# Performance work log

Hardware: AMD Instinct MI355X
Metric: run time of the kernel (lower is better)

## Reference

```python
import jax, jax.numpy as jnp
import numpy as np

N_HEADS = 12
HEAD_DIM = 64
EMB_DIM = 768
ATTN_DIM = N_HEADS * HEAD_DIM


def setup_inputs() -> dict:
    key = jax.random.key(0)
    k1, k2, k3, k4 = jax.random.split(key, 4)
    B, N = 8, 1024
    x = jax.random.normal(k1, (B, N, EMB_DIM), dtype=jnp.float32)
    scale = 1.0 / np.sqrt(EMB_DIM)
    w_qkv = jax.random.normal(k2, (EMB_DIM, 3 * ATTN_DIM), dtype=jnp.float32) * scale
    w_out = jax.random.normal(k3, (ATTN_DIM, EMB_DIM), dtype=jnp.float32) * (1.0 / np.sqrt(ATTN_DIM))
    b_out = jax.random.normal(k4, (EMB_DIM,), dtype=jnp.float32) * 0.01
    return {"x": x, "w_qkv": w_qkv, "w_out": w_out, "b_out": b_out}


def reference(x, w_qkv, w_out, b_out):
    B, N, _ = x.shape
    qkv = jnp.einsum('bnd,de->bne', x, w_qkv)  # [B,N,3*attn_dim]
    q, k, v = jnp.split(qkv, 3, axis=-1)
    # [B, n_heads, N, head_dim]
    def heads(t):
        return t.reshape(B, N, N_HEADS, HEAD_DIM).transpose(0, 2, 1, 3)
    q, k, v = heads(q), heads(k), heads(v)
    scores = jnp.einsum('bhnd,bhmd->bhnm', q, k) * (HEAD_DIM ** -0.5)
    attn = jax.nn.softmax(scores, axis=-1)
    out = jnp.einsum('bhnm,bhmd->bhnd', attn, v)
    out = out.transpose(0, 2, 1, 3).reshape(B, N, ATTN_DIM)
    return jnp.einsum('bnd,de->bne', out, w_out) + b_out
```

## Files before the change

kernel.cpp:

```cpp
#include <hip/hip_runtime.h>
#include <hip/hip_bf16.h>

typedef unsigned short u16;
typedef __attribute__((ext_vector_type(8))) short short8;
typedef __attribute__((ext_vector_type(4))) float floatx4;

#define SEQ    1024
#define EMB    768
#define NHEADS 12
#define HDIM   64
#define QKVD   2304
#define BATCH  8
#define ROWS   8192
#define QKW    1536

__device__ __forceinline__ u16 f2bf(float f) {
  unsigned int x; __builtin_memcpy(&x, &f, 4);
  x = (x + 0x7FFFu + ((x >> 16) & 1u)) >> 16;
  return (u16)x;
}
__device__ __forceinline__ unsigned int pack2bf_t(float a, float b) {
  unsigned int ua, ub;
  __builtin_memcpy(&ua, &a, 4); __builtin_memcpy(&ub, &b, 4);
  return (ub & 0xFFFF0000u) | (ua >> 16);
}

__device__ __forceinline__ void gld16(const void* g, void* l) {
  __builtin_amdgcn_global_load_lds(
      (const __attribute__((address_space(1))) void*)g,
      (__attribute__((address_space(3))) void*)l, 16, 0, 0);
}

#define PIPE_BARRIER_VM(N) asm volatile("s_waitcnt vmcnt(" #N ")\n\ts_barrier" ::: "memory")
#define PIPE_BARRIER       asm volatile("s_barrier" ::: "memory")

__global__ __launch_bounds__(256) void prep(const float* __restrict__ x,
                                            const float* __restrict__ wqkv,
                                            const float* __restrict__ wout,
                                            u16* __restrict__ xb,
                                            u16* __restrict__ dqkv,
                                            u16* __restrict__ dout) {
  const int t = threadIdx.x;
  if (blockIdx.x < 3072) {
    const int i = (blockIdx.x * 256 + t) * 8;
    u16 tmp[8];
#pragma unroll
    for (int j = 0; j < 8; ++j) tmp[j] = f2bf(x[i + j]);
    *(uint4*)(xb + i) = *(const uint4*)tmp;
    return;
  }
  __shared__ u16 tile[32][33];
  const int bid = blockIdx.x - 3072;
  const int bx = bid % 96, by = bid / 96;
  const bool second = bx >= 72;
  const float* in = second ? wout : wqkv;
  u16* out = second ? dout : dqkv;
  const int C = second ? EMB : QKVD;
  const int c0 = (second ? bx - 72 : bx) * 32, r0 = by * 32;
  const int tx = t & 31, ty = t >> 5;
#pragma unroll
  for (int i = 0; i < 4; ++i)
    tile[ty + i * 8][tx] = f2bf(in[(size_t)(r0 + ty + i * 8) * C + c0 + tx]);
  __syncthreads();
#pragma unroll
  for (int i = 0; i < 4; ++i)
    out[(size_t)(c0 + ty + i * 8) * EMB + r0 + tx] = tile[tx][ty + i * 8];
}

__global__ __launch_bounds__(256) void gemm_qkv(const u16* __restrict__ A,
                                                const u16* __restrict__ Bt,
                                                u16* __restrict__ qk,
                                                u16* __restrict__ vT) {
  constexpr int K = EMB, ITERS = K / 64;
  __shared__ __align__(16) u16 As[2][128 * 64];
  __shared__ __align__(16) u16 Bs[2][128 * 64];
  const int t = threadIdx.x;
  const int w = t >> 6, lane = t & 63, l16 = lane & 15, quad = lane >> 4;
  const int wm = (w >> 1) * 64, wn = (w & 1) * 64;
  const int flat = blockIdx.y * 18 + blockIdx.x;
  const int grp = flat / 144, loc = flat % 144;
  const int m0 = (grp * 8 + (loc & 7)) * 128;
  const int n0 = (loc >> 3) * 128;

  auto stage = [&](int k0, int buf) {
#pragma unroll
    for (int i = 0; i < 4; ++i) {
      const int idx = i * 256 + t;
      const int row = idx >> 3;
      const int gc8 = (((idx & 7) ^ (row & 7)) << 3);
      gld16(A  + (size_t)(m0 + row) * K + k0 + gc8, &As[buf][(size_t)idx * 8]);
      gld16(Bt + (size_t)(n0 + row) * K + k0 + gc8, &Bs[buf][(size_t)idx * 8]);
    }
  };

  floatx4 acc[4][4];
#pragma unroll
  for (int mt = 0; mt < 4; ++mt)
#pragma unroll
    for (int nt = 0; nt < 4; ++nt) acc[mt][nt] = (floatx4){0.f, 0.f, 0.f, 0.f};

  stage(0, 0);
#pragma unroll
  for (int it = 0; it < ITERS; ++it) {
    const int cur = it & 1;
    if (it + 1 < ITERS) {
      stage((it + 1) * 64, cur ^ 1);
      PIPE_BARRIER_VM(8);
    } else {
      PIPE_BARRIER_VM(0);
    }
#pragma unroll
    for (int kk = 0; kk < 2; ++kk) {
      short8 a[4], b[4];
#pragma unroll
      for (int mt = 0; mt < 4; ++mt) {
        const int row = wm + mt * 16 + l16;
        a[mt] = *(const short8*)(&As[cur][row * 64 + ((((kk << 2) + quad) ^ (row & 7)) << 3)]);
      }
#pragma unroll
      for (int nt = 0; nt < 4; ++nt) {
        const int row = wn + nt * 16 + l16;
        b[nt] = *(const short8*)(&Bs[cur][row * 64 + ((((kk << 2) + quad) ^ (row & 7)) << 3)]);
      }
#pragma unroll
      for (int mt = 0; mt < 4; ++mt)
#pragma unroll
        for (int nt = 0; nt < 4; ++nt)
          acc[mt][nt] = __builtin_amdgcn_mfma_f32_16x16x32_bf16(a[mt], b[nt], acc[mt][nt], 0, 0, 0);
    }
    PIPE_BARRIER;
  }

  if (n0 < QKW) {
    const float qs = (n0 < EMB) ? 0.1803368801111f : 1.0f;
#pragma unroll
    for (int mt = 0; mt < 4; ++mt)
#pragma unroll
      for (int nt = 0; nt < 4; ++nt) {
        const int col = n0 + wn + nt * 16 + l16;
#pragma unroll
        for (int r = 0; r < 4; ++r) {
          const int row = m0 + wm + mt * 16 + quad * 4 + r;
          qk[(size_t)row * QKW + col] = f2bf(acc[mt][nt][r] * qs);
        }
      }
  } else {
#pragma unroll
    for (int mt = 0; mt < 4; ++mt) {
      const int rowb = m0 + wm + mt * 16 + quad * 4;
      const int b = rowb >> 10, n = rowb & 1023;
#pragma unroll
      for (int nt = 0; nt < 4; ++nt) {
        const int vc = n0 + wn + nt * 16 + l16 - QKW;
        const int h = vc >> 6, d = vc & 63;
        ushort4 pk;
        pk.x = f2bf(acc[mt][nt][0]); pk.y = f2bf(acc[mt][nt][1]);
        pk.z = f2bf(acc[mt][nt][2]); pk.w = f2bf(acc[mt][nt][3]);
        *(ushort4*)(vT + ((size_t)(b * NHEADS + h) * HDIM + d) * SEQ + n) = pk;
      }
    }
  }
}

__global__ __launch_bounds__(256) void flash_attn(const u16* __restrict__ qk,
                                                  const u16* __restrict__ vT,
                                                  u16* __restrict__ aout) {
  __shared__ __align__(16) u16 Ks[2][64 * 64];
  __shared__ __align__(16) u16 Vs[2][64 * 64];

  const int t = threadIdx.x;
  const int w = t >> 6, lane = t & 63, l16 = lane & 15, quad = lane >> 4;
  const int bh = blockIdx.x, b = bh / NHEADS, h = bh % NHEADS;
  const int m0 = blockIdx.y * 128;
  constexpr int ITERS = SEQ / 64;
  const int swz = l16 & 7;

  const size_t kbase = (size_t)(b * SEQ) * QKW + EMB + h * HDIM;
  const size_t vbase = (size_t)bh * HDIM * SEQ;

  auto stage = [&](int n0, int buf) {
#pragma unroll
    for (int i = 0; i < 2; ++i) {
      const int idx = i * 256 + t, r = idx >> 3;
      const int gc = (((idx & 7) ^ (r & 7)) << 3);
      gld16(qk + kbase + (size_t)(n0 + r) * QKW + gc, &Ks[buf][(size_t)idx * 8]);
      gld16(vT + vbase + (size_t)r * SEQ + n0 + gc,   &Vs[buf][(size_t)idx * 8]);
    }
  };

  short8 bq[2][2];
  const u16* qrow = qk + (size_t)(b * SEQ + m0 + w * 32 + l16) * QKW + h * HDIM;
#pragma unroll
  for (int mt = 0; mt < 2; ++mt)
#pragma unroll
    for (int kc = 0; kc < 2; ++kc)
      bq[mt][kc] = *(const short8*)(qrow + (size_t)mt * 16 * QKW + kc * 32 + quad * 8);

  stage(0, 0);

  short8 ones;
#pragma unroll
  for (int j = 0; j < 8; ++j) ones[j] = (short)0x3F80;
  const floatx4 zf = (floatx4){0.f, 0.f, 0.f, 0.f};

  floatx4 o[2][4], lcc[2];
#pragma unroll
  for (int mt = 0; mt < 2; ++mt) {
    lcc[mt] = zf;
#pragma unroll
    for (int dt = 0; dt < 4; ++dt) o[mt][dt] = zf;
  }

#pragma unroll
  for (int it = 0; it < ITERS; ++it) {
    const int cur = it & 1;
    if (it + 1 < ITERS) {
      stage((it + 1) * 64, cur ^ 1);
      PIPE_BARRIER_VM(4);
    } else {
      PIPE_BARRIER_VM(0);
    }

    floatx4 st[4][2];
#pragma unroll
    for (int kt = 0; kt < 4; ++kt) {
      const int krow = (kt * 16 + l16) * 64;
      const short8 ak0 = *(const short8*)(&Ks[cur][krow + ((quad ^ swz) << 3)]);
      const short8 ak1 = *(const short8*)(&Ks[cur][krow + (((4 + quad) ^ swz) << 3)]);
#pragma unroll
      for (int mt = 0; mt < 2; ++mt) {
        st[kt][mt] = __builtin_amdgcn_mfma_f32_16x16x32_bf16(ak0, bq[mt][0], zf, 0, 0, 0);
        st[kt][mt] = __builtin_amdgcn_mfma_f32_16x16x32_bf16(ak1, bq[mt][1], st[kt][mt], 0, 0, 0);
      }
    }

    union { uint4 u; short8 s; } bp[2][2];
#pragma unroll
    for (int mt = 0; mt < 2; ++mt)
#pragma unroll
      for (int ktp = 0; ktp < 2; ++ktp) {
        const floatx4 e0 = st[2 * ktp][mt], e1 = st[2 * ktp + 1][mt];
        bp[ktp][mt].u.x = pack2bf_t(__builtin_amdgcn_exp2f(e0[0]), __builtin_amdgcn_exp2f(e0[1]));
        bp[ktp][mt].u.y = pack2bf_t(__builtin_amdgcn_exp2f(e0[2]), __builtin_amdgcn_exp2f(e0[3]));
        bp[ktp][mt].u.z = pack2bf_t(__builtin_amdgcn_exp2f(e1[0]), __builtin_amdgcn_exp2f(e1[1]));
        bp[ktp][mt].u.w = pack2bf_t(__builtin_amdgcn_exp2f(e1[2]), __builtin_amdgcn_exp2f(e1[3]));
      }

#pragma unroll
    for (int ktp = 0; ktp < 2; ++ktp) {
      const int gl = 4 * ktp + (quad >> 1), ho = (quad & 1) * 4;
#pragma unroll
      for (int dt = 0; dt < 4; ++dt) {
        const int row = dt * 16 + l16;
        const u16* vr = &Vs[cur][row * 64];
        union { uint4 u; short8 s; } av;
        const uint2 lo = *(const uint2*)(vr + ((gl ^ swz) << 3) + ho);
        const uint2 hi = *(const uint2*)(vr + (((gl + 2) ^ swz) << 3) + ho);
        av.u.x = lo.x; av.u.y = lo.y; av.u.z = hi.x; av.u.w = hi.y;
#pragma unroll
        for (int mt = 0; mt < 2; ++mt)
          o[mt][dt] = __builtin_amdgcn_mfma_f32_16x16x32_bf16(av.s, bp[ktp][mt].s, o[mt][dt], 0, 0, 0);
      }
#pragma unroll
      for (int mt = 0; mt < 2; ++mt)
        lcc[mt] = __builtin_amdgcn_mfma_f32_16x16x32_bf16(ones, bp[ktp][mt].s, lcc[mt], 0, 0, 0);
    }
    PIPE_BARRIER;
  }

#pragma unroll
  for (int mt = 0; mt < 2; ++mt) {
    const float inv = 1.f / lcc[mt][0];
    const size_t arow = (size_t)(b * SEQ + m0 + w * 32 + mt * 16 + l16) * EMB + h * HDIM;
#pragma unroll
    for (int dt = 0; dt < 4; ++dt) {
      ushort4 pk;
      pk.x = f2bf(o[mt][dt][0] * inv); pk.y = f2bf(o[mt][dt][1] * inv);
      pk.z = f2bf(o[mt][dt][2] * inv); pk.w = f2bf(o[mt][dt][3] * inv);
      *(ushort4*)(aout + arow + dt * 16 + quad * 4) = pk;
    }
  }
}

__global__ __launch_bounds__(256) void gemm_out(const u16* __restrict__ A,
                                                const u16* __restrict__ Bt,
                                                const float* __restrict__ bias,
                                                float* __restrict__ C) {
  constexpr int K = EMB, N = EMB, ITERS = K / 64;
  __shared__ __align__(16) u16 As[2][64 * 64];
  __shared__ __align__(16) u16 Bs[2][128 * 64];
  const int t = threadIdx.x;
  const int w = t >> 6, lane = t & 63, l16 = lane & 15, quad = lane >> 4;
  const int wm = (w >> 1) * 32, wn = (w & 1) * 64;
  const int flat = blockIdx.y * 6 + blockIdx.x;
  const int grp = flat / 48, loc = flat % 48;
  const int m0 = (grp * 8 + (loc & 7)) * 64;
  const int n0 = (loc >> 3) * 128;

  auto stage = [&](int k0, int buf) {
#pragma unroll
    for (int i = 0; i < 2; ++i) {
      const int idx = i * 256 + t;
      const int row = idx >> 3;
      const int gc8 = (((idx & 7) ^ (row & 7)) << 3);
      gld16(A + (size_t)(m0 + row) * K + k0 + gc8, &As[buf][(size_t)idx * 8]);
    }
#pragma unroll
    for (int i = 0; i < 4; ++i) {
      const int idx = i * 256 + t;
      const int row = idx >> 3;
      const int gc8 = (((idx & 7) ^ (row & 7)) << 3);
      gld16(Bt + (size_t)(n0 + row) * K + k0 + gc8, &Bs[buf][(size_t)idx * 8]);
    }
  };

  floatx4 acc[2][4];
#pragma unroll
  for (int mt = 0; mt < 2; ++mt)
#pragma unroll
    for (int nt = 0; nt < 4; ++nt) acc[mt][nt] = (floatx4){0.f, 0.f, 0.f, 0.f};

  stage(0, 0);
#pragma unroll
  for (int it = 0; it < ITERS; ++it) {
    const int cur = it & 1;
    if (it + 1 < ITERS) {
      stage((it + 1) * 64, cur ^ 1);
      PIPE_BARRIER_VM(6);
    } else {
      PIPE_BARRIER_VM(0);
    }
#pragma unroll
    for (int kk = 0; kk < 2; ++kk) {
      short8 a[2], b[4];
#pragma unroll
      for (int mt = 0; mt < 2; ++mt) {
        const int row = wm + mt * 16 + l16;
        a[mt] = *(const short8*)(&As[cur][row * 64 + ((((kk << 2) + quad) ^ (row & 7)) << 3)]);
      }
#pragma unroll
      for (int nt = 0; nt < 4; ++nt) {
        const int row = wn + nt * 16 + l16;
        b[nt] = *(const short8*)(&Bs[cur][row * 64 + ((((kk << 2) + quad) ^ (row & 7)) << 3)]);
      }
#pragma unroll
      for (int mt = 0; mt < 2; ++mt)
#pragma unroll
        for (int nt = 0; nt < 4; ++nt)
          acc[mt][nt] = __builtin_amdgcn_mfma_f32_16x16x32_bf16(a[mt], b[nt], acc[mt][nt], 0, 0, 0);
    }
    PIPE_BARRIER;
  }

#pragma unroll
  for (int mt = 0; mt < 2; ++mt)
#pragma unroll
    for (int nt = 0; nt < 4; ++nt) {
      const int col = n0 + wn + nt * 16 + l16;
      const float badd = bias[col];
#pragma unroll
      for (int r = 0; r < 4; ++r) {
        const int row = m0 + wm + mt * 16 + quad * 4 + r;
        C[(size_t)row * N + col] = acc[mt][nt][r] + badd;
      }
    }
}

extern "C" void kernel_launch(void* const* d_in, const int* in_sizes, int n_in,
                              void* d_out, int out_size, void* d_ws, size_t ws_size,
                              hipStream_t stream) {
  const float* x     = (const float*)d_in[0];
  const float* w_qkv = (const float*)d_in[1];
  const float* w_out = (const float*)d_in[2];
  const float* b_out = (const float*)d_in[3];
  float* out = (float*)d_out;

  u16* qk    = (u16*)d_ws;
  u16* vT    = qk    + (size_t)ROWS * QKW;
  u16* xb    = vT    + (size_t)BATCH * NHEADS * HDIM * SEQ;
  u16* aout  = xb;
  u16* wqkvT = xb    + (size_t)ROWS * EMB;
  u16* woutT = wqkvT + (size_t)QKVD * EMB;

  prep<<<3072 + 2304, 256, 0, stream>>>(x, w_qkv, w_out, xb, wqkvT, woutT);

  gemm_qkv<<<dim3(18, 64), 256, 0, stream>>>(xb, wqkvT, qk, vT);

  flash_attn<<<dim3(BATCH * NHEADS, SEQ / 128), 256, 0, stream>>>(qk, vT, aout);

  gemm_out<<<dim3(6, 128), 256, 0, stream>>>(aout, woutT, b_out, out);
}
```

Before: 170.4 us.

## Split flash attention KV tile across two wave groups with LDS reduction

The flash attention block grows from 4 to 8 waves. The two groups of four waves each handle half of every 64-key tile and share the same Q rows, and the staging load is spread over 512 threads. At the end, partial O and row sums from the second group are written to shared memory and added by the first group before normalization. This aims to raise wave count and latency hiding per CU, at the cost of an extra LDS reduction and barriers, plus duplicated Q loads and softmax-free exp work per wave.

```diff
diff --git a/kernel.cpp b/kernel.cpp
--- a/kernel.cpp
+++ b/kernel.cpp
@@ -162,14 +162,15 @@
   }
 }
 
-__global__ __launch_bounds__(256) void flash_attn(const u16* __restrict__ qk,
-                                                  const u16* __restrict__ vT,
-                                                  u16* __restrict__ aout) {
-  __shared__ __align__(16) u16 Ks[2][64 * 64];
-  __shared__ __align__(16) u16 Vs[2][64 * 64];
+__global__ __launch_bounds__(512, 6) void flash_attn(const u16* __restrict__ qk,
+                                                     const u16* __restrict__ vT,
+                                                     u16* __restrict__ aout) {
+  __shared__ __align__(16) u16 smemKV[4][64 * 64];
 
   const int t = threadIdx.x;
   const int w = t >> 6, lane = t & 63, l16 = lane & 15, quad = lane >> 4;
+  const int pw = w & 3;
+  const int kh = w >> 2;
   const int bh = blockIdx.x, b = bh / NHEADS, h = bh % NHEADS;
   const int m0 = blockIdx.y * 128;
   constexpr int ITERS = SEQ / 64;
@@ -179,17 +180,14 @@
   const size_t vbase = (size_t)bh * HDIM * SEQ;
 
   auto stage = [&](int n0, int buf) {
-#pragma unroll
-    for (int i = 0; i < 2; ++i) {
-      const int idx = i * 256 + t, r = idx >> 3;
-      const int gc = (((idx & 7) ^ (r & 7)) << 3);
-      gld16(qk + kbase + (size_t)(n0 + r) * QKW + gc, &Ks[buf][(size_t)idx * 8]);
-      gld16(vT + vbase + (size_t)r * SEQ + n0 + gc,   &Vs[buf][(size_t)idx * 8]);
-    }
+    const int r = t >> 3;
+    const int gc = (((t & 7) ^ (r & 7)) << 3);
+    gld16(qk + kbase + (size_t)(n0 + r) * QKW + gc, &smemKV[buf][(size_t)t * 8]);
+    gld16(vT + vbase + (size_t)r * SEQ + n0 + gc,   &smemKV[2 + buf][(size_t)t * 8]);
   };
 
   short8 bq[2][2];
-  const u16* qrow = qk + (size_t)(b * SEQ + m0 + w * 32 + l16) * QKW + h * HDIM;
+  const u16* qrow = qk + (size_t)(b * SEQ + m0 + pw * 32 + l16) * QKW + h * HDIM;
 #pragma unroll
   for (int mt = 0; mt < 2; ++mt)
 #pragma unroll
@@ -216,68 +214,81 @@
     const int cur = it & 1;
     if (it + 1 < ITERS) {
       stage((it + 1) * 64, cur ^ 1);
-      PIPE_BARRIER_VM(4);
+      PIPE_BARRIER_VM(2);
     } else {
       PIPE_BARRIER_VM(0);
     }
 
-    floatx4 st[4][2];
-#pragma unroll
-    for (int kt = 0; kt < 4; ++kt) {
-      const int krow = (kt * 16 + l16) * 64;
-      const short8 ak0 = *(const short8*)(&Ks[cur][krow + ((quad ^ swz) << 3)]);
-      const short8 ak1 = *(const short8*)(&Ks[cur][krow + (((4 + quad) ^ swz) << 3)]);
+    floatx4 st[2][2];
+#pragma unroll
+    for (int kt2 = 0; kt2 < 2; ++kt2) {
+      const int krow = ((2 * kh + kt2) * 16 + l16) * 64;
+      const short8 ak0 = *(const short8*)(&smemKV[cur][krow + ((quad ^ swz) << 3)]);
+      const short8 ak1 = *(const short8*)(&smemKV[cur][krow + (((4 + quad) ^ swz) << 3)]);
 #pragma unroll
       for (int mt = 0; mt < 2; ++mt) {
-        st[kt][mt] = __builtin_amdgcn_mfma_f32_16x16x32_bf16(ak0, bq[mt][0], zf, 0, 0, 0);
-        st[kt][mt] = __builtin_amdgcn_mfma_f32_16x16x32_bf16(ak1, bq[mt][1], st[kt][mt], 0, 0, 0);
-      }
-    }
-
-    union { uint4 u; short8 s; } bp[2][2];
-#pragma unroll
-    for (int mt = 0; mt < 2; ++mt)
-#pragma unroll
-      for (int ktp = 0; ktp < 2; ++ktp) {
-        const floatx4 e0 = st[2 * ktp][mt], e1 = st[2 * ktp + 1][mt];
-        bp[ktp][mt].u.x = pack2bf_t(__builtin_amdgcn_exp2f(e0[0]), __builtin_amdgcn_exp2f(e0[1]));
-        bp[ktp][mt].u.y = pack2bf_t(__builtin_amdgcn_exp2f(e0[2]), __builtin_amdgcn_exp2f(e0[3]));
-        bp[ktp][mt].u.z = pack2bf_t(__builtin_amdgcn_exp2f(e1[0]), __builtin_amdgcn_exp2f(e1[1]));
-        bp[ktp][mt].u.w = pack2bf_t(__builtin_amdgcn_exp2f(e1[2]), __builtin_amdgcn_exp2f(e1[3]));
-      }
-
-#pragma unroll
-    for (int ktp = 0; ktp < 2; ++ktp) {
-      const int gl = 4 * ktp + (quad >> 1), ho = (quad & 1) * 4;
+        st[kt2][mt] = __builtin_amdgcn_mfma_f32_16x16x32_bf16(ak0, bq[mt][0], zf, 0, 0, 0);
+        st[kt2][mt] = __builtin_amdgcn_mfma_f32_16x16x32_bf16(ak1, bq[mt][1], st[kt2][mt], 0, 0, 0);
+      }
+    }
+
+    union { uint4 u; short8 s; } bp[2];
+#pragma unroll
+    for (int mt = 0; mt < 2; ++mt) {
+      const floatx4 e0 = st[0][mt], e1 = st[1][mt];
+      bp[mt].u.x = pack2bf_t(__builtin_amdgcn_exp2f(e0[0]), __builtin_amdgcn_exp2f(e0[1]));
+      bp[mt].u.y = pack2bf_t(__builtin_amdgcn_exp2f(e0[2]), __builtin_amdgcn_exp2f(e0[3]));
+      bp[mt].u.z = pack2bf_t(__builtin_amdgcn_exp2f(e1[0]), __builtin_amdgcn_exp2f(e1[1]));
+      bp[mt].u.w = pack2bf_t(__builtin_amdgcn_exp2f(e1[2]), __builtin_amdgcn_exp2f(e1[3]));
+    }
+
+    {
+      const int gl = 4 * kh + (quad >> 1), ho = (quad & 1) * 4;
 #pragma unroll
       for (int dt = 0; dt < 4; ++dt) {
         const int row = dt * 16 + l16;
-        const u16* vr = &Vs[cur][row * 64];
+        const u16* vr = &smemKV[2 + cur][row * 64];
         union { uint4 u; short8 s; } av;
         const uint2 lo = *(const uint2*)(vr + ((gl ^ swz) << 3) + ho);
         const uint2 hi = *(const uint2*)(vr + (((gl + 2) ^ swz) << 3) + ho);
         av.u.x = lo.x; av.u.y = lo.y; av.u.z = hi.x; av.u.w = hi.y;
 #pragma unroll
         for (int mt = 0; mt < 2; ++mt)
-          o[mt][dt] = __builtin_amdgcn_mfma_f32_16x16x32_bf16(av.s, bp[ktp][mt].s, o[mt][dt], 0, 0, 0);
+          o[mt][dt] = __builtin_amdgcn_mfma_f32_16x16x32_bf16(av.s, bp[mt].s, o[mt][dt], 0, 0, 0);
       }
 #pragma unroll
       for (int mt = 0; mt < 2; ++mt)
-        lcc[mt] = __builtin_amdgcn_mfma_f32_16x16x32_bf16(ones, bp[ktp][mt].s, lcc[mt], 0, 0, 0);
+        lcc[mt] = __builtin_amdgcn_mfma_f32_16x16x32_bf16(ones, bp[mt].s, lcc[mt], 0, 0, 0);
     }
     PIPE_BARRIER;
   }
 
+  float* cb = (float*)&smemKV[0][0];
 #pragma unroll
   for (int mt = 0; mt < 2; ++mt) {
-    const float inv = 1.f / lcc[mt][0];
-    const size_t arow = (size_t)(b * SEQ + m0 + w * 32 + mt * 16 + l16) * EMB + h * HDIM;
-#pragma unroll
-    for (int dt = 0; dt < 4; ++dt) {
-      ushort4 pk;
-      pk.x = f2bf(o[mt][dt][0] * inv); pk.y = f2bf(o[mt][dt][1] * inv);
-      pk.z = f2bf(o[mt][dt][2] * inv); pk.w = f2bf(o[mt][dt][3] * inv);
-      *(ushort4*)(aout + arow + dt * 16 + quad * 4) = pk;
+    __syncthreads();
+    if (kh == 1) {
+      float* dst = cb + (size_t)(pw * 64 + lane) * 17;
+#pragma unroll
+      for (int dt = 0; dt < 4; ++dt)
+#pragma unroll
+        for (int r = 0; r < 4; ++r) dst[dt * 4 + r] = o[mt][dt][r];
+      dst[16] = lcc[mt][0];
+    }
+    __syncthreads();
+    if (kh == 0) {
+      const float* src = cb + (size_t)(pw * 64 + lane) * 17;
+      const float inv = 1.f / (lcc[mt][0] + src[16]);
+      const size_t arow = (size_t)(b * SEQ + m0 + pw * 32 + mt * 16 + l16) * EMB + h * HDIM;
+#pragma unroll
+      for (int dt = 0; dt < 4; ++dt) {
+        ushort4 pk;
+        pk.x = f2bf((o[mt][dt][0] + src[dt * 4 + 0]) * inv);
+        pk.y = f2bf((o[mt][dt][1] + src[dt * 4 + 1]) * inv);
+        pk.z = f2bf((o[mt][dt][2] + src[dt * 4 + 2]) * inv);
+        pk.w = f2bf((o[mt][dt][3] + src[dt * 4 + 3]) * inv);
+        *(ushort4*)(aout + arow + dt * 16 + quad * 4) = pk;
+      }
     }
   }
 }
@@ -386,7 +397,7 @@
 
   gemm_qkv<<<dim3(18, 64), 256, 0, stream>>>(xb, wqkvT, qk, vT);
 
-  flash_attn<<<dim3(BATCH * NHEADS, SEQ / 128), 256, 0, stream>>>(qk, vT, aout);
+  flash_attn<<<dim3(BATCH * NHEADS, SEQ / 128), 512, 0, stream>>>(qk, vT, aout);
 
   gemm_out<<<dim3(6, 128), 256, 0, stream>>>(aout, woutT, b_out, out);
 }
```

Result: slower. 330.0 us (+93.7%).

## Load K/V directly from global in flash attention, drop LDS staging

Applied to the files above, without the earlier changes.

The flash-attention kernel no longer stages K and V tiles through double-buffered shared memory with async global-to-LDS loads and block barriers. Each wavefront now reads its K and V fragments straight from global memory, relying on L1/L2 caching, and the loop is left un-unrolled. This removes LDS traffic and per-iteration barriers, but the four waves in a block now fetch the same K/V data separately and there is no prefetch to hide global latency. The GEMM kernels also gain an explicit lgkmcnt wait before each loop-end barrier.

```diff
diff --git a/kernel.cpp b/kernel.cpp
--- a/kernel.cpp
+++ b/kernel.cpp
@@ -32,7 +32,7 @@
 }
 
 #define PIPE_BARRIER_VM(N) asm volatile("s_waitcnt vmcnt(" #N ")\n\ts_barrier" ::: "memory")
-#define PIPE_BARRIER       asm volatile("s_barrier" ::: "memory")
+#define PIPE_BARRIER_LG    asm volatile("s_waitcnt lgkmcnt(0)\n\ts_barrier" ::: "memory")
 
 __global__ __launch_bounds__(256) void prep(const float* __restrict__ x,
                                             const float* __restrict__ wqkv,
@@ -128,7 +128,7 @@
         for (int nt = 0; nt < 4; ++nt)
           acc[mt][nt] = __builtin_amdgcn_mfma_f32_16x16x32_bf16(a[mt], b[nt], acc[mt][nt], 0, 0, 0);
     }
-    PIPE_BARRIER;
+    PIPE_BARRIER_LG;
   }
 
   if (n0 < QKW) {
@@ -165,39 +165,22 @@
 __global__ __launch_bounds__(256) void flash_attn(const u16* __restrict__ qk,
                                                   const u16* __restrict__ vT,
                                                   u16* __restrict__ aout) {
-  __shared__ __align__(16) u16 Ks[2][64 * 64];
-  __shared__ __align__(16) u16 Vs[2][64 * 64];
-
   const int t = threadIdx.x;
   const int w = t >> 6, lane = t & 63, l16 = lane & 15, quad = lane >> 4;
   const int bh = blockIdx.x, b = bh / NHEADS, h = bh % NHEADS;
-  const int m0 = blockIdx.y * 128;
-  constexpr int ITERS = SEQ / 64;
-  const int swz = l16 & 7;
-
-  const size_t kbase = (size_t)(b * SEQ) * QKW + EMB + h * HDIM;
-  const size_t vbase = (size_t)bh * HDIM * SEQ;
-
-  auto stage = [&](int n0, int buf) {
-#pragma unroll
-    for (int i = 0; i < 2; ++i) {
-      const int idx = i * 256 + t, r = idx >> 3;
-      const int gc = (((idx & 7) ^ (r & 7)) << 3);
-      gld16(qk + kbase + (size_t)(n0 + r) * QKW + gc, &Ks[buf][(size_t)idx * 8]);
-      gld16(vT + vbase + (size_t)r * SEQ + n0 + gc,   &Vs[buf][(size_t)idx * 8]);
-    }
-  };
+  const int m0 = blockIdx.y * 128 + w * 32;
+
+  const u16* kbase = qk + (size_t)(b * SEQ) * QKW + EMB + h * HDIM;
+  const u16* vbase = vT + (size_t)bh * HDIM * SEQ;
 
   short8 bq[2][2];
-  const u16* qrow = qk + (size_t)(b * SEQ + m0 + w * 32 + l16) * QKW + h * HDIM;
+  const u16* qrow = qk + (size_t)(b * SEQ + m0 + l16) * QKW + h * HDIM;
 #pragma unroll
   for (int mt = 0; mt < 2; ++mt)
 #pragma unroll
     for (int kc = 0; kc < 2; ++kc)
       bq[mt][kc] = *(const short8*)(qrow + (size_t)mt * 16 * QKW + kc * 32 + quad * 8);
 
-  stage(0, 0);
-
   short8 ones;
 #pragma unroll
   for (int j = 0; j < 8; ++j) ones[j] = (short)0x3F80;
@@ -211,22 +194,14 @@
     for (int dt = 0; dt < 4; ++dt) o[mt][dt] = zf;
   }
 
-#pragma unroll
-  for (int it = 0; it < ITERS; ++it) {
-    const int cur = it & 1;
-    if (it + 1 < ITERS) {
-      stage((it + 1) * 64, cur ^ 1);
-      PIPE_BARRIER_VM(4);
-    } else {
-      PIPE_BARRIER_VM(0);
-    }
-
+#pragma unroll 1
+  for (int n0 = 0; n0 < SEQ; n0 += 64) {
     floatx4 st[4][2];
 #pragma unroll
     for (int kt = 0; kt < 4; ++kt) {
-      const int krow = (kt * 16 + l16) * 64;
-      const short8 ak0 = *(const short8*)(&Ks[cur][krow + ((quad ^ swz) << 3)]);
-      const short8 ak1 = *(const short8*)(&Ks[cur][krow + (((4 + quad) ^ swz) << 3)]);
+      const u16* kr = kbase + (size_t)(n0 + kt * 16 + l16) * QKW;
+      const short8 ak0 = *(const short8*)(kr + quad * 8);
+      const short8 ak1 = *(const short8*)(kr + 32 + quad * 8);
 #pragma unroll
       for (int mt = 0; mt < 2; ++mt) {
         st[kt][mt] = __builtin_amdgcn_mfma_f32_16x16x32_bf16(ak0, bq[mt][0], zf, 0, 0, 0);
@@ -248,14 +223,12 @@
 
 #pragma unroll
     for (int ktp = 0; ktp < 2; ++ktp) {
-      const int gl = 4 * ktp + (quad >> 1), ho = (quad & 1) * 4;
 #pragma unroll
       for (int dt = 0; dt < 4; ++dt) {
-        const int row = dt * 16 + l16;
-        const u16* vr = &Vs[cur][row * 64];
+        const u16* vr = vbase + (size_t)(dt * 16 + l16) * SEQ + n0 + 32 * ktp + quad * 4;
         union { uint4 u; short8 s; } av;
-        const uint2 lo = *(const uint2*)(vr + ((gl ^ swz) << 3) + ho);
-        const uint2 hi = *(const uint2*)(vr + (((gl + 2) ^ swz) << 3) + ho);
+        const uint2 lo = *(const uint2*)(vr);
+        const uint2 hi = *(const uint2*)(vr + 16);
         av.u.x = lo.x; av.u.y = lo.y; av.u.z = hi.x; av.u.w = hi.y;
 #pragma unroll
         for (int mt = 0; mt < 2; ++mt)
@@ -265,13 +238,12 @@
       for (int mt = 0; mt < 2; ++mt)
         lcc[mt] = __builtin_amdgcn_mfma_f32_16x16x32_bf16(ones, bp[ktp][mt].s, lcc[mt], 0, 0, 0);
     }
-    PIPE_BARRIER;
   }
 
 #pragma unroll
   for (int mt = 0; mt < 2; ++mt) {
     const float inv = 1.f / lcc[mt][0];
-    const size_t arow = (size_t)(b * SEQ + m0 + w * 32 + mt * 16 + l16) * EMB + h * HDIM;
+    const size_t arow = (size_t)(b * SEQ + m0 + mt * 16 + l16) * EMB + h * HDIM;
 #pragma unroll
     for (int dt = 0; dt < 4; ++dt) {
       ushort4 pk;
@@ -349,7 +321,7 @@
         for (int nt = 0; nt < 4; ++nt)
           acc[mt][nt] = __builtin_amdgcn_mfma_f32_16x16x32_bf16(a[mt], b[nt], acc[mt][nt], 0, 0, 0);
     }
-    PIPE_BARRIER;
+    PIPE_BARRIER_LG;
   }
 
 #pragma unroll
```

After: 268.4 us. +57.5%, slower.
